# Kernel tuning notes

Measured on AMD Instinct MI355X. Metric: run time of the kernel, lower is better.

The kernel has to match this reference:

```python
import jax, jax.numpy as jnp
import numpy as np

N, P, C, K = 1024, 64, 64, 16
C_MID, C_OUT = 128, 128


def setup_inputs() -> dict:
    key = jax.random.key(0)
    k1, k2, k3, k4 = jax.random.split(key, 4)
    x = jax.random.normal(k1, (N, P, C), dtype=jnp.float32)
    mask = jnp.zeros((N, P), dtype=bool)  # True = padded particle
    # Conv2d(2C -> C_MID, 1x1, no bias); Conv2d(C_MID -> C_OUT, 1x1, no bias)
    W1 = jax.random.normal(k2, (C_MID, 2 * C), dtype=jnp.float32) * 0.05
    W2 = jax.random.normal(k3, (C_OUT, C_MID), dtype=jnp.float32) * 0.05
    # Conv1d(C -> C_OUT, kernel 1, no bias) residual path
    Wres = jax.random.normal(k4, (C_OUT, C), dtype=jnp.float32) * 0.05
    return {"x": x, "mask": mask, "W1": W1, "W2": W2, "Wres": Wres}


def reference(x, mask, W1, W2, Wres):
    n, p, c = x.shape
    k = K
    # residual: Conv1d kernel-1 == per-particle matmul  (N,P,C)->(N,P,C_OUT)
    x_res = jnp.einsum('npc,oc->npo', x, Wres)
    # direction = x with padded rows set to +inf (mask all False here)
    direction = jnp.where(mask[..., None], jnp.inf, x)
    # pairwise L2 distance over channel dim: (N,P,P)
    diff = direction[:, :, None, :] - direction[:, None, :, :]
    dist = jnp.sqrt(jnp.sum(diff * diff, axis=-1))
    # smallest K+1 distances, drop self
    _, idx = jax.lax.top_k(-dist, k + 1)
    knn = idx[..., 1:]  # (N,P,K)
    # faithful to torch: gather along the CHANNEL dim with particle indices
    f_center = jnp.broadcast_to(x[:, :, None, :], (n, p, k, c))  # (N,P,K,C)
    f_neighbor = jnp.take_along_axis(f_center, knn[..., None], axis=-1)  # (N,P,K,1)
    feat = jnp.concatenate([f_center, f_center - f_neighbor], axis=-1)  # (N,P,K,2C)
    # 1x1 conv MLP (channels-last layout)
    h = jax.nn.relu(jnp.einsum('npkc,oc->npko', feat, W1))
    h = jax.nn.relu(jnp.einsum('npkc,oc->npko', h, W2))  # (N,P,K,C_OUT)
    # mask neighbors pointing at padded slots, masked mean over K
    n_valid = p - jnp.sum(mask, axis=-1)  # (N,)
    mask_K = knn >= n_valid[:, None, None]  # (N,P,K) bool
    h = jnp.where(mask_K[..., None], 0.0, h)
    denom = (k - jnp.sum(mask_K, axis=-1)).astype(h.dtype)  # (N,P)
    agg = jnp.sum(h, axis=2) / denom[..., None]  # (N,P,C_OUT)
    return jax.nn.relu(agg + x_res)
```

## Files before the change

kernel.cpp:

```cpp
#include <hip/hip_runtime.h>
#include <hip/hip_bf16.h>

typedef __bf16 bf16x8 __attribute__((ext_vector_type(8)));
typedef float  f32x4  __attribute__((ext_vector_type(4)));
typedef unsigned long long u64;

#define MFMA_BF16 __builtin_amdgcn_mfma_f32_16x16x32_bf16

#define WS_W2P  (1u << 20)
#define WS_WCP  ((1u << 20) + 32768u)
#define WS_SSUM ((1u << 20) + 65536u)

#define K1_XS   0
#define K1_SD   17408
#define K1_SQ   34048
#define K1_LDS  38144

__global__ __launch_bounds__(256, 3)
void knn_kernel(const float* __restrict__ x, const float* __restrict__ W1,
                const float* __restrict__ W2, const float* __restrict__ Wres,
                unsigned* __restrict__ ws)
{
    __shared__ char smem[K1_LDS];
    float*    xs   = (float*)(smem + K1_XS);
    float*    sd_t = (float*)(smem + K1_SD);
    unsigned* sqp  = (unsigned*)(smem + K1_SQ);

    const int tid = threadIdx.x;
    const int n   = blockIdx.x;
    const float* __restrict__ xn = x + (size_t)n * 4096;

    #pragma unroll
    for (int i = 0; i < 4; ++i) {
        int e4 = tid + 256 * i;
        f32x4 v = *(const f32x4*)(xn + e4 * 4);
        int row = e4 >> 4, col = (e4 & 15) * 4;
        float* dst = xs + row * 68 + col;
        dst[0] = v[0]; dst[1] = v[1]; dst[2] = v[2]; dst[3] = v[3];
    }
    __syncthreads();

    {
#pragma clang fp contract(off)
        const int p = tid >> 2, rb = tid & 3;
        f32x4 xp4[16];
        const f32x4* xprow = (const f32x4*)(xs + p * 68);
        #pragma unroll
        for (int v = 0; v < 16; ++v) xp4[v] = xprow[v];
        u64 keys[16];
        #pragma unroll
        for (int i = 0; i < 16; ++i) {
            const int q = 4 * i + rb;
            const f32x4* xq4 = (const f32x4*)(xs + q * 68);
            f32x4 d0 = xp4[0] - xq4[0];
            f32x4 d1 = xp4[1] - xq4[1];
            f32x4 rA = d0 * d0;
            f32x4 rB = d1 * d1;
            #pragma unroll
            for (int b = 1; b < 8; ++b) {
                f32x4 e0 = xp4[2*b]   - xq4[2*b];   rA = rA + e0 * e0;
                f32x4 e1 = xp4[2*b+1] - xq4[2*b+1]; rB = rB + e1 * e1;
            }
            float d2 = ((rA[0]+rA[1]) + (rA[2]+rA[3])) + ((rB[0]+rB[1]) + (rB[2]+rB[3]));
            float key = sqrtf(d2);
            unsigned kb = __float_as_uint(key);
            if (q == p) kb = 0x7f800000u;
            keys[i] = ((u64)kb << 8) | (unsigned)q;
        }
        #pragma unroll
        for (int pp = 1; pp < 16; pp <<= 1) {
            #pragma unroll
            for (int k = pp; k >= 1; k >>= 1) {
                #pragma unroll
                for (int j = k & (pp - 1); j + k < 16; j += 2 * k) {
                    #pragma unroll
                    for (int i = 0; i < k; ++i) {
                        if (i + j + k < 16 && ((i + j) / (2 * pp) == (i + j + k) / (2 * pp))) {
                            u64 a = keys[i + j], b = keys[i + j + k];
                            u64 lo = a < b ? a : b;
                            u64 hi = a < b ? b : a;
                            keys[i + j] = lo; keys[i + j + k] = hi;
                        }
                    }
                }
            }
        }
        #pragma unroll
        for (int t = 0; t < 4; ++t) {
            unsigned wq = 0;
            #pragma unroll
            for (int b = 0; b < 4; ++b) {
                int s = 4 * t + b;
                sd_t[(rb * 16 + s) * 65 + p] = __uint_as_float((unsigned)(keys[s] >> 8));
                wq |= ((unsigned)(keys[s] & 0x3fu)) << (8 * b);
            }
            sqp[(rb * 4 + t) * 64 + p] = wq;
        }
    }
    __syncthreads();

    if (tid < 64) {
        const int p = tid;
        float dh[4]; unsigned qh[4]; int ix[4];
        #pragma unroll
        for (int b = 0; b < 4; ++b) {
            ix[b] = 0;
            dh[b] = sd_t[(b * 16) * 65 + p];
            qh[b] = sqp[(b * 4) * 64 + p] & 63u;
        }
        unsigned knacc[4] = {0u, 0u, 0u, 0u};
        for (int s = 0; s < 16; ++s) {
            int bsel = 0; float bd = dh[0]; unsigned bq = qh[0];
            #pragma unroll
            for (int b = 1; b < 4; ++b) {
                bool t = (dh[b] < bd) || (dh[b] == bd && qh[b] < bq);
                if (t) { bd = dh[b]; bq = qh[b]; bsel = b; }
            }
            knacc[s >> 2] |= bq << ((s & 3) * 8);
            int ni = ix[bsel] + 1; ix[bsel] = ni;
            int nc = ni < 15 ? ni : 15;
            float nd = sd_t[(bsel * 16 + nc) * 65 + p];
            unsigned nw = sqp[(bsel * 4 + (nc >> 2)) * 64 + p];
            unsigned nq = (nw >> ((nc & 3) * 8)) & 63u;
            if (ni > 15) nd = __builtin_inff();
            dh[bsel] = nd; qh[bsel] = nq;
        }
        *(uint4*)(ws + (size_t)n * 256 + p * 4) =
            make_uint4(knacc[0], knacc[1], knacc[2], knacc[3]);
    }

    if (n < 32) {
        if (tid < 64) {
            const int l = tid, f = n;
            int ntl = f >> 2, kt = f & 3;
            int o = ntl * 16 + (l & 15);
            int c = kt * 32 + (l >> 4) * 8;
            const float* s0 = W2 + o * 128 + c;
            f32x4 a0 = *(const f32x4*)s0, a1 = *(const f32x4*)(s0 + 4);
            bf16x8 fr;
            fr[0]=(__bf16)a0[0]; fr[1]=(__bf16)a0[1]; fr[2]=(__bf16)a0[2]; fr[3]=(__bf16)a0[3];
            fr[4]=(__bf16)a1[0]; fr[5]=(__bf16)a1[1]; fr[6]=(__bf16)a1[2]; fr[7]=(__bf16)a1[3];
            *(bf16x8*)((__bf16*)((char*)ws + WS_W2P) + (size_t)(f * 64 + l) * 8) = fr;
        }
    } else if (n < 64) {
        if (tid < 64) {
            const int l = tid, f = n - 32;
            int wv = f >> 3, rem = f & 7, ntl = rem >> 1, kt = rem & 1;
            int o = wv * 64 + ntl * 16 + (l & 15);
            int c = kt * 32 + (l >> 4) * 8;
            float v[8];
            if (o < 128) {
                const float* s0 = W1 + o * 128 + c;
                f32x4 a0 = *(const f32x4*)s0,      a1 = *(const f32x4*)(s0 + 4);
                f32x4 b0 = *(const f32x4*)(s0+64), b1 = *(const f32x4*)(s0 + 68);
                v[0]=a0[0]+b0[0]; v[1]=a0[1]+b0[1]; v[2]=a0[2]+b0[2]; v[3]=a0[3]+b0[3];
                v[4]=a1[0]+b1[0]; v[5]=a1[1]+b1[1]; v[6]=a1[2]+b1[2]; v[7]=a1[3]+b1[3];
            } else {
                const float* s0 = Wres + (o - 128) * 64 + c;
                f32x4 a0 = *(const f32x4*)s0, a1 = *(const f32x4*)(s0 + 4);
                v[0]=a0[0]; v[1]=a0[1]; v[2]=a0[2]; v[3]=a0[3];
                v[4]=a1[0]; v[5]=a1[1]; v[6]=a1[2]; v[7]=a1[3];
            }
            bf16x8 fr;
            #pragma unroll
            for (int j = 0; j < 8; ++j) fr[j] = (__bf16)v[j];
            *(bf16x8*)((__bf16*)((char*)ws + WS_WCP) + (size_t)(f * 64 + l) * 8) = fr;
        }
    } else if (n == 64) {
        if (tid < 128) {
            const f32x4* src = (const f32x4*)(W1 + tid * 128 + 64);
            f32x4 a = {0.f, 0.f, 0.f, 0.f};
            #pragma unroll
            for (int i = 0; i < 16; ++i) a += src[i];
            ((float*)((char*)ws + WS_SSUM))[tid] = a[0] + a[1] + a[2] + a[3];
        }
    }
}

#define K2_UB   0
#define K2_XR   16384
#define K2_SS   32768
#define K2_LDS  33280

__global__ __launch_bounds__(256, 2)
void gemm_kernel(const float* __restrict__ x, const unsigned* __restrict__ ws,
                 float* __restrict__ out)
{
    __shared__ char smem[K2_LDS];
    __bf16*   ub   = (__bf16*)(smem + K2_UB);
    __bf16*   xres = (__bf16*)(smem + K2_XR);
    float*    Ssum = (float*)(smem + K2_SS);

    const __bf16* __restrict__ w2p   = (const __bf16*)((const char*)ws + WS_W2P);
    const __bf16* __restrict__ wcp   = (const __bf16*)((const char*)ws + WS_WCP);
    const float*  __restrict__ ssums = (const float*)((const char*)ws + WS_SSUM);

    const int tid  = threadIdx.x;
    const int lane = tid & 63;
    const int w    = tid >> 6;
    const int lm   = lane & 15;
    const int lq   = lane >> 4;
    const int n    = blockIdx.x;
    const float* __restrict__ xn = x + (size_t)n * 4096;

    float sval[16];
    {
        const unsigned* kb = ws + (size_t)n * 256;
        unsigned jw[16];
        #pragma unroll
        for (int pi = 0; pi < 16; ++pi) {
            int p = w + pi * 4;
            jw[pi] = kb[p * 4 + (lm >> 2)];
        }
        #pragma unroll
        for (int pi = 0; pi < 16; ++pi) {
            int p = w + pi * 4;
            int j = (int)((jw[pi] >> ((lm & 3) * 8)) & 63u);
            sval[pi] = xn[p * 64 + j];
        }
    }

    if (tid < 128) Ssum[tid] = ssums[tid];

    {
        bf16x8 wcf[4][2];
        #pragma unroll
        for (int ntl = 0; ntl < 4; ++ntl) {
            #pragma unroll
            for (int kt = 0; kt < 2; ++kt)
                wcf[ntl][kt] = *(const bf16x8*)(wcp + (size_t)((w * 8 + ntl * 2 + kt) * 64 + lane) * 8);
        }
        #pragma unroll
        for (int mt = 0; mt < 4; ++mt) {
            bf16x8 af[2];
            #pragma unroll
            for (int kt = 0; kt < 2; ++kt) {
                const float* arow = xn + (mt * 16 + lm) * 64 + kt * 32 + lq * 8;
                f32x4 a0 = *(const f32x4*)arow, a1 = *(const f32x4*)(arow + 4);
                bf16x8 f;
                f[0]=(__bf16)a0[0]; f[1]=(__bf16)a0[1]; f[2]=(__bf16)a0[2]; f[3]=(__bf16)a0[3];
                f[4]=(__bf16)a1[0]; f[5]=(__bf16)a1[1]; f[6]=(__bf16)a1[2]; f[7]=(__bf16)a1[3];
                af[kt] = f;
            }
            #pragma unroll
            for (int ntl = 0; ntl < 4; ++ntl) {
                f32x4 acc = {0.f, 0.f, 0.f, 0.f};
                acc = MFMA_BF16(af[0], wcf[ntl][0], acc, 0, 0, 0);
                acc = MFMA_BF16(af[1], wcf[ntl][1], acc, 0, 0, 0);
                int o = w * 64 + ntl * 16 + lm;
                #pragma unroll
                for (int r = 0; r < 4; ++r) {
                    int p = mt * 16 + lq * 4 + r;
                    if (o < 128) ub[p * 128 + o] = (__bf16)acc[r];
                    else         xres[p * 128 + (o - 128)] = (__bf16)acc[r];
                }
            }
        }
    }
    __syncthreads();

    {
        bf16x8 w2f[8][4];
        #pragma unroll
        for (int ntl = 0; ntl < 8; ++ntl) {
            #pragma unroll
            for (int kt = 0; kt < 4; ++kt)
                w2f[ntl][kt] = *(const bf16x8*)(w2p + (size_t)((ntl * 4 + kt) * 64 + lane) * 8);
        }
        float ss[4][8];
        #pragma unroll
        for (int kt = 0; kt < 4; ++kt) {
            #pragma unroll
            for (int e = 0; e < 8; ++e) ss[kt][e] = Ssum[kt * 32 + lq * 8 + e];
        }
        const size_t outbase = (size_t)n * 8192;
        const int c0 = lq * 32 + lm;

        bf16x8 upv_n[4];
        float  xr0_n, xr1_n;
        {
            const int p0 = w;
            #pragma unroll
            for (int kt = 0; kt < 4; ++kt)
                upv_n[kt] = *(const bf16x8*)(ub + p0 * 128 + kt * 32 + lq * 8);
            xr0_n = (float)xres[p0 * 128 + c0];
            xr1_n = (float)xres[p0 * 128 + c0 + 16];
        }

        #pragma unroll 1
        for (int pi = 0; pi < 16; ++pi) {
            const int p = w + pi * 4;
            bf16x8 upv[4];
            #pragma unroll
            for (int kt = 0; kt < 4; ++kt) upv[kt] = upv_n[kt];
            const float xr0 = xr0_n, xr1 = xr1_n;

            if (pi < 15) {
                const int pn = p + 4;
                #pragma unroll
                for (int kt = 0; kt < 4; ++kt)
                    upv_n[kt] = *(const bf16x8*)(ub + pn * 128 + kt * 32 + lq * 8);
                xr0_n = (float)xres[pn * 128 + c0];
                xr1_n = (float)xres[pn * 128 + c0 + 16];
            }

            const float sv_p = sval[pi];
            f32x4 acc[8];
            #pragma unroll
            for (int ntl = 0; ntl < 8; ++ntl) acc[ntl] = f32x4{0.f, 0.f, 0.f, 0.f};
            #pragma unroll
            for (int kt = 0; kt < 4; ++kt) {
                bf16x8 af;
                #pragma unroll
                for (int e = 0; e < 8; ++e) {
                    float h = fmaf(-sv_p, ss[kt][e], (float)upv[kt][e]);
                    af[e] = (__bf16)fmaxf(h, 0.0f);
                }
                #pragma unroll
                for (int ntl = 0; ntl < 8; ++ntl)
                    acc[ntl] = MFMA_BF16(af, w2f[ntl][kt], acc[ntl], 0, 0, 0);
            }
            float sv[8];
            #pragma unroll
            for (int ntl = 0; ntl < 8; ++ntl) {
                float part = fmaxf(acc[ntl][0], 0.f) + fmaxf(acc[ntl][1], 0.f)
                           + fmaxf(acc[ntl][2], 0.f) + fmaxf(acc[ntl][3], 0.f);
                part += __shfl_xor(part, 16);
                part += __shfl_xor(part, 32);
                sv[ntl] = part;
            }
            float r0 = sv[0], r1 = sv[1];
            if (lq == 1) { r0 = sv[2]; r1 = sv[3]; }
            if (lq == 2) { r0 = sv[4]; r1 = sv[5]; }
            if (lq == 3) { r0 = sv[6]; r1 = sv[7]; }
            out[outbase + p * 128 + c0]      = fmaxf(r0 * 0.0625f + xr0, 0.0f);
            out[outbase + p * 128 + c0 + 16] = fmaxf(r1 * 0.0625f + xr1, 0.0f);
        }
    }
}

extern "C" void kernel_launch(void* const* d_in, const int* in_sizes, int n_in,
                              void* d_out, int out_size, void* d_ws, size_t ws_size,
                              hipStream_t stream) {
    const float* x    = (const float*)d_in[0];
    const float* W1   = (const float*)d_in[2];
    const float* W2   = (const float*)d_in[3];
    const float* Wres = (const float*)d_in[4];
    float* outp = (float*)d_out;
    unsigned* ws = (unsigned*)d_ws;
    int nblocks = in_sizes[0] / 4096;
    hipLaunchKernelGGL(knn_kernel,  dim3(nblocks), dim3(256), 0, stream,
                       x, W1, W2, Wres, ws);
    hipLaunchKernelGGL(gemm_kernel, dim3(nblocks), dim3(256), 0, stream,
                       x, ws, outp);
}
```

Before: 161.1 us.

## Process two samples per gemm block and use a butterfly reduction across lanes

```diff
diff --git a/kernel.cpp b/kernel.cpp
--- a/kernel.cpp
+++ b/kernel.cpp
@@ -178,9 +178,9 @@
 }
 
 #define K2_UB   0
-#define K2_XR   16384
-#define K2_SS   32768
-#define K2_LDS  33280
+#define K2_XR   32768
+#define K2_SS   65536
+#define K2_LDS  66048
 
 __global__ __launch_bounds__(256, 2)
 void gemm_kernel(const float* __restrict__ x, const unsigned* __restrict__ ws,
@@ -200,25 +200,7 @@
     const int w    = tid >> 6;
     const int lm   = lane & 15;
     const int lq   = lane >> 4;
-    const int n    = blockIdx.x;
-    const float* __restrict__ xn = x + (size_t)n * 4096;
-
-    float sval[16];
-    {
-        const unsigned* kb = ws + (size_t)n * 256;
-        unsigned jw[16];
-        #pragma unroll
-        for (int pi = 0; pi < 16; ++pi) {
-            int p = w + pi * 4;
-            jw[pi] = kb[p * 4 + (lm >> 2)];
-        }
-        #pragma unroll
-        for (int pi = 0; pi < 16; ++pi) {
-            int p = w + pi * 4;
-            int j = (int)((jw[pi] >> ((lm & 3) * 8)) & 63u);
-            sval[pi] = xn[p * 64 + j];
-        }
-    }
+    const int n0   = blockIdx.x * 2;
 
     if (tid < 128) Ssum[tid] = ssums[tid];
 
@@ -231,28 +213,34 @@
                 wcf[ntl][kt] = *(const bf16x8*)(wcp + (size_t)((w * 8 + ntl * 2 + kt) * 64 + lane) * 8);
         }
         #pragma unroll
-        for (int mt = 0; mt < 4; ++mt) {
-            bf16x8 af[2];
-            #pragma unroll
-            for (int kt = 0; kt < 2; ++kt) {
-                const float* arow = xn + (mt * 16 + lm) * 64 + kt * 32 + lq * 8;
-                f32x4 a0 = *(const f32x4*)arow, a1 = *(const f32x4*)(arow + 4);
-                bf16x8 f;
-                f[0]=(__bf16)a0[0]; f[1]=(__bf16)a0[1]; f[2]=(__bf16)a0[2]; f[3]=(__bf16)a0[3];
-                f[4]=(__bf16)a1[0]; f[5]=(__bf16)a1[1]; f[6]=(__bf16)a1[2]; f[7]=(__bf16)a1[3];
-                af[kt] = f;
-            }
-            #pragma unroll
-            for (int ntl = 0; ntl < 4; ++ntl) {
-                f32x4 acc = {0.f, 0.f, 0.f, 0.f};
-                acc = MFMA_BF16(af[0], wcf[ntl][0], acc, 0, 0, 0);
-                acc = MFMA_BF16(af[1], wcf[ntl][1], acc, 0, 0, 0);
-                int o = w * 64 + ntl * 16 + lm;
-                #pragma unroll
-                for (int r = 0; r < 4; ++r) {
-                    int p = mt * 16 + lq * 4 + r;
-                    if (o < 128) ub[p * 128 + o] = (__bf16)acc[r];
-                    else         xres[p * 128 + (o - 128)] = (__bf16)acc[r];
+        for (int ns = 0; ns < 2; ++ns) {
+            const float* xn = x + (size_t)(n0 + ns) * 4096;
+            __bf16* ubn = ub   + ns * 8192;
+            __bf16* xrn = xres + ns * 8192;
+            #pragma unroll
+            for (int mt = 0; mt < 4; ++mt) {
+                bf16x8 af[2];
+                #pragma unroll
+                for (int kt = 0; kt < 2; ++kt) {
+                    const float* arow = xn + (mt * 16 + lm) * 64 + kt * 32 + lq * 8;
+                    f32x4 a0 = *(const f32x4*)arow, a1 = *(const f32x4*)(arow + 4);
+                    bf16x8 f;
+                    f[0]=(__bf16)a0[0]; f[1]=(__bf16)a0[1]; f[2]=(__bf16)a0[2]; f[3]=(__bf16)a0[3];
+                    f[4]=(__bf16)a1[0]; f[5]=(__bf16)a1[1]; f[6]=(__bf16)a1[2]; f[7]=(__bf16)a1[3];
+                    af[kt] = f;
+                }
+                #pragma unroll
+                for (int ntl = 0; ntl < 4; ++ntl) {
+                    f32x4 acc = {0.f, 0.f, 0.f, 0.f};
+                    acc = MFMA_BF16(af[0], wcf[ntl][0], acc, 0, 0, 0);
+                    acc = MFMA_BF16(af[1], wcf[ntl][1], acc, 0, 0, 0);
+                    int o = w * 64 + ntl * 16 + lm;
+                    #pragma unroll
+                    for (int r = 0; r < 4; ++r) {
+                        int p = mt * 16 + lq * 4 + r;
+                        if (o < 128) ubn[p * 128 + o] = (__bf16)acc[r];
+                        else         xrn[p * 128 + (o - 128)] = (__bf16)acc[r];
+                    }
                 }
             }
         }
@@ -273,68 +261,66 @@
             #pragma unroll
             for (int e = 0; e < 8; ++e) ss[kt][e] = Ssum[kt * 32 + lq * 8 + e];
         }
-        const size_t outbase = (size_t)n * 8192;
         const int c0 = lq * 32 + lm;
 
-        bf16x8 upv_n[4];
-        float  xr0_n, xr1_n;
-        {
-            const int p0 = w;
-            #pragma unroll
-            for (int kt = 0; kt < 4; ++kt)
-                upv_n[kt] = *(const bf16x8*)(ub + p0 * 128 + kt * 32 + lq * 8);
-            xr0_n = (float)xres[p0 * 128 + c0];
-            xr1_n = (float)xres[p0 * 128 + c0 + 16];
-        }
-
         #pragma unroll 1
-        for (int pi = 0; pi < 16; ++pi) {
-            const int p = w + pi * 4;
-            bf16x8 upv[4];
-            #pragma unroll
-            for (int kt = 0; kt < 4; ++kt) upv[kt] = upv_n[kt];
-            const float xr0 = xr0_n, xr1 = xr1_n;
-
-            if (pi < 15) {
-                const int pn = p + 4;
-                #pragma unroll
-                for (int kt = 0; kt < 4; ++kt)
-                    upv_n[kt] = *(const bf16x8*)(ub + pn * 128 + kt * 32 + lq * 8);
-                xr0_n = (float)xres[pn * 128 + c0];
-                xr1_n = (float)xres[pn * 128 + c0 + 16];
-            }
-
-            const float sv_p = sval[pi];
-            f32x4 acc[8];
-            #pragma unroll
-            for (int ntl = 0; ntl < 8; ++ntl) acc[ntl] = f32x4{0.f, 0.f, 0.f, 0.f};
-            #pragma unroll
-            for (int kt = 0; kt < 4; ++kt) {
-                bf16x8 af;
-                #pragma unroll
-                for (int e = 0; e < 8; ++e) {
-                    float h = fmaf(-sv_p, ss[kt][e], (float)upv[kt][e]);
-                    af[e] = (__bf16)fmaxf(h, 0.0f);
-                }
-                #pragma unroll
-                for (int ntl = 0; ntl < 8; ++ntl)
-                    acc[ntl] = MFMA_BF16(af, w2f[ntl][kt], acc[ntl], 0, 0, 0);
-            }
-            float sv[8];
-            #pragma unroll
-            for (int ntl = 0; ntl < 8; ++ntl) {
-                float part = fmaxf(acc[ntl][0], 0.f) + fmaxf(acc[ntl][1], 0.f)
-                           + fmaxf(acc[ntl][2], 0.f) + fmaxf(acc[ntl][3], 0.f);
-                part += __shfl_xor(part, 16);
-                part += __shfl_xor(part, 32);
-                sv[ntl] = part;
-            }
-            float r0 = sv[0], r1 = sv[1];
-            if (lq == 1) { r0 = sv[2]; r1 = sv[3]; }
-            if (lq == 2) { r0 = sv[4]; r1 = sv[5]; }
-            if (lq == 3) { r0 = sv[6]; r1 = sv[7]; }
-            out[outbase + p * 128 + c0]      = fmaxf(r0 * 0.0625f + xr0, 0.0f);
-            out[outbase + p * 128 + c0 + 16] = fmaxf(r1 * 0.0625f + xr1, 0.0f);
+        for (int ns = 0; ns < 2; ++ns) {
+            const float*    xn  = x + (size_t)(n0 + ns) * 4096;
+            const unsigned* kb  = ws + (size_t)(n0 + ns) * 256;
+            const __bf16*   ubn = ub   + ns * 8192;
+            const __bf16*   xrn = xres + ns * 8192;
+            const size_t outbase = (size_t)(n0 + ns) * 8192;
+
+            #pragma unroll 1
+            for (int pi = 0; pi < 16; ++pi) {
+                const int p = w + pi * 4;
+                unsigned jw = kb[p * 4 + (lm >> 2)];
+                int   j     = (int)((jw >> ((lm & 3) * 8)) & 63u);
+                float sv_p  = xn[p * 64 + j];
+
+                f32x4 acc[8];
+                #pragma unroll
+                for (int ntl = 0; ntl < 8; ++ntl) acc[ntl] = f32x4{0.f, 0.f, 0.f, 0.f};
+                #pragma unroll
+                for (int kt = 0; kt < 4; ++kt) {
+                    bf16x8 upv = *(const bf16x8*)(ubn + p * 128 + kt * 32 + lq * 8);
+                    bf16x8 af;
+                    #pragma unroll
+                    for (int e = 0; e < 8; ++e) {
+                        float h = fmaf(-sv_p, ss[kt][e], (float)upv[e]);
+                        af[e] = (__bf16)fmaxf(h, 0.0f);
+                    }
+                    #pragma unroll
+                    for (int ntl = 0; ntl < 8; ++ntl)
+                        acc[ntl] = MFMA_BF16(af, w2f[ntl][kt], acc[ntl], 0, 0, 0);
+                }
+                float part[8];
+                #pragma unroll
+                for (int ntl = 0; ntl < 8; ++ntl) {
+                    part[ntl] = fmaxf(acc[ntl][0], 0.f) + fmaxf(acc[ntl][1], 0.f)
+                              + fmaxf(acc[ntl][2], 0.f) + fmaxf(acc[ntl][3], 0.f);
+                }
+                float s1[4];
+                #pragma unroll
+                for (int i = 0; i < 4; ++i) {
+                    float mine = (lq < 2) ? part[i] : part[4 + i];
+                    float thr  = (lq < 2) ? part[4 + i] : part[i];
+                    s1[i] = mine + __shfl_xor(thr, 32);
+                }
+                float r0, r1;
+                {
+                    float m0 = ((lq & 1) == 0) ? s1[0] : s1[2];
+                    float m1 = ((lq & 1) == 0) ? s1[1] : s1[3];
+                    float t0 = ((lq & 1) == 0) ? s1[2] : s1[0];
+                    float t1 = ((lq & 1) == 0) ? s1[3] : s1[1];
+                    r0 = m0 + __shfl_xor(t0, 16);
+                    r1 = m1 + __shfl_xor(t1, 16);
+                }
+                float x0 = (float)xrn[p * 128 + c0];
+                float x1 = (float)xrn[p * 128 + c0 + 16];
+                out[outbase + p * 128 + c0]      = fmaxf(r0 * 0.0625f + x0, 0.0f);
+                out[outbase + p * 128 + c0 + 16] = fmaxf(r1 * 0.0625f + x1, 0.0f);
+            }
         }
     }
 }
@@ -351,6 +337,6 @@
     int nblocks = in_sizes[0] / 4096;
     hipLaunchKernelGGL(knn_kernel,  dim3(nblocks), dim3(256), 0, stream,
                        x, W1, W2, Wres, ws);
-    hipLaunchKernelGGL(gemm_kernel, dim3(nblocks), dim3(256), 0, stream,
+    hipLaunchKernelGGL(gemm_kernel, dim3(nblocks / 2), dim3(256), 0, stream,
                        x, ws, outp);
 }
```

New measurement: 155.5 us. 3.5% less time.
